# Optimization experiments

Hardware: AMD Instinct MI355X
Metric: run time of the kernel (lower is better)

The kernel has to match this reference:

```python
import jax, jax.numpy as jnp
import numpy as np

# ---- 4-wire quantum gate: RX(x_w + theta_w) per wire, CNOT ring, <Z_w> per wire ----
N_WIRES = 4
DIM = 2 ** N_WIRES  # 16 statevector amplitudes

def _cnot_perm_inv():
    # CNOTs (0,1),(1,2),(2,3),(3,0) applied sequentially permute computational basis states.
    # inv[j] = k such that basis state k maps to j; then psi_new = psi_old[inv].
    inv = np.zeros(DIM, dtype=np.int32)
    for k in range(DIM):
        b = [(k >> 3) & 1, (k >> 2) & 1, (k >> 1) & 1, k & 1]  # wire 0 = MSB
        b[1] ^= b[0]; b[2] ^= b[1]; b[3] ^= b[2]; b[0] ^= b[3]
        nk = (b[0] << 3) | (b[1] << 2) | (b[2] << 1) | b[3]
        inv[nk] = k
    return jnp.asarray(inv)

_PERM = _cnot_perm_inv()
# sign[k, w] = (-1)^{bit_w(k)} for PauliZ expectation on wire w
_ZSIGN = jnp.asarray(np.array([[1.0 - 2.0 * ((k >> (3 - w)) & 1) for w in range(N_WIRES)]
                               for k in range(DIM)], dtype=np.float32))  # [16, 4]

def _qgate(angles, theta):
    # angles: [B, 4]. Encoder RX(x_w) then trainable RX(theta_w) on the same wire = RX(x_w + theta_w).
    a = (angles + theta) * 0.5
    c, s = jnp.cos(a), jnp.sin(a)
    amp = jnp.stack([c + 0j, (-1j) * s], axis=-1)  # [B, 4, 2] per-wire RX|0> amplitudes
    # product state over 4 wires -> [B, 16]
    psi = jnp.einsum('bi,bj,bk,bl->bijkl', amp[:, 0], amp[:, 1], amp[:, 2], amp[:, 3]).reshape(-1, DIM)
    psi = psi[:, _PERM]  # CNOT ring (classical basis permutation)
    probs = jnp.real(psi * jnp.conj(psi))  # [B, 16]
    return probs @ _ZSIGN  # [B, 4] PauliZ expectations


def setup_inputs() -> dict:
    key = jax.random.key(0)
    T, B, D, H, Q = 256, 2048, 128, 4, 4
    ks = jax.random.split(key, 16)
    inp = {"inputs": jax.random.normal(ks[0], (T, B, D), dtype=jnp.float32)}
    bound = 1.0 / float(np.sqrt(D + H))  # torch Linear default init range
    for j, n in enumerate(["f", "i", "u", "o"]):
        inp["W" + n] = jax.random.uniform(ks[1 + j], (Q, D + H), jnp.float32, -bound, bound)
        inp["b" + n] = jax.random.uniform(ks[5 + j], (Q,), jnp.float32, -bound, bound)
        inp["th" + n] = jax.random.normal(ks[9 + j], (Q,), dtype=jnp.float32)  # trainable RX angles
    return inp


def reference(inputs, Wf, bf, Wi, bi, Wu, bu, Wo, bo, thf, thi, thu, tho):
    B = inputs.shape[1]
    H = N_WIRES  # hidden_dim == n_qubits == 4
    h0 = jnp.zeros((B, H), dtype=inputs.dtype)
    c0 = jnp.zeros((B, H), dtype=inputs.dtype)

    def step(carry, x):
        hx, cx = carry
        comb = jnp.concatenate([x, hx], axis=1)  # [B, D+H]
        f = jax.nn.sigmoid(_qgate(comb @ Wf.T + bf, thf))
        i = jax.nn.sigmoid(_qgate(comb @ Wi.T + bi, thi))
        g = jnp.tanh(_qgate(comb @ Wu.T + bu, thu))
        o = jax.nn.sigmoid(_qgate(comb @ Wo.T + bo, tho))
        cx = f * cx + i * g
        hx = o * jnp.tanh(cx)
        return (hx, cx), hx

    (hx, cx), stacked = jax.lax.scan(step, (h0, c0), inputs)
    return (stacked, hx, cx)
```

## Files before the change

kernel.cpp:

```cpp
#include <hip/hip_runtime.h>

#define TT 256
#define BB 2048
#define DIN 128
#define DWROW 132
#define INV2PI 0.15915494309189535f
#define LOG2E  1.4426950408889634f

__device__ __forceinline__ const float* rfl_ptr(const float* p) {
    unsigned long long u = (unsigned long long)p;
    unsigned lo = __builtin_amdgcn_readfirstlane((unsigned)u);
    unsigned hi = __builtin_amdgcn_readfirstlane((unsigned)(u >> 32));
    return (const float*)(((unsigned long long)hi << 32) | lo);
}

__device__ __forceinline__ float bperm(int byte_addr, float v) {
    return __int_as_float(__builtin_amdgcn_ds_bpermute(byte_addr, __float_as_int(v)));
}

__global__ __launch_bounds__(256) void qlstm_phase1(
    const float* __restrict__ x,
    const float* __restrict__ Wf, const float* __restrict__ bf, const float* __restrict__ thf,
    const float* __restrict__ Wi, const float* __restrict__ bi, const float* __restrict__ thi,
    const float* __restrict__ Wu, const float* __restrict__ bu, const float* __restrict__ thu,
    const float* __restrict__ Wo, const float* __restrict__ bo, const float* __restrict__ tho,
    float* __restrict__ Ax)
{
    __shared__ float xT[DIN][65];

    const int tid = threadIdx.x;
    const size_t tile = blockIdx.x;

    const float4* xg = (const float4*)x + tile * (64 * DIN / 4);
#pragma unroll
    for (int i = 0; i < 8; ++i) {
        int f   = i * 256 + tid;
        int row = f >> 5;
        int c4  = f & 31;
        float4 v = xg[f];
        xT[4 * c4 + 0][row] = v.x;
        xT[4 * c4 + 1][row] = v.y;
        xT[4 * c4 + 2][row] = v.z;
        xT[4 * c4 + 3][row] = v.w;
    }
    __syncthreads();

    const int wv   = tid >> 6;
    const int lane = tid & 63;

    const float* Wp  = (wv == 0) ? Wf  : (wv == 1) ? Wi  : (wv == 2) ? Wu  : Wo;
    const float* bp  = (wv == 0) ? bf  : (wv == 1) ? bi  : (wv == 2) ? bu  : bo;
    const float* thp = (wv == 0) ? thf : (wv == 1) ? thi : (wv == 2) ? thu : tho;
    const float* Wg  = rfl_ptr(Wp);
    const float* bg  = rfl_ptr(bp);
    const float* thg = rfl_ptr(thp);

    float acc0 = bg[0] + thg[0];
    float acc1 = bg[1] + thg[1];
    float acc2 = bg[2] + thg[2];
    float acc3 = bg[3] + thg[3];

#pragma unroll 8
    for (int j = 0; j < DIN; ++j) {
        float xv = xT[j][lane];
        acc0 = fmaf(xv, Wg[0 * DWROW + j], acc0);
        acc1 = fmaf(xv, Wg[1 * DWROW + j], acc1);
        acc2 = fmaf(xv, Wg[2 * DWROW + j], acc2);
        acc3 = fmaf(xv, Wg[3 * DWROW + j], acc3);
    }

    float4 o;
    o.x = acc0 * INV2PI; o.y = acc1 * INV2PI;
    o.z = acc2 * INV2PI; o.w = acc3 * INV2PI;
    ((float4*)Ax)[(tile * 64 + lane) * 4 + wv] = o;
}

__global__ __launch_bounds__(64) void qlstm_phase2(
    const float* __restrict__ Ax,
    const float* __restrict__ Wf, const float* __restrict__ Wi,
    const float* __restrict__ Wu, const float* __restrict__ Wo,
    float* __restrict__ out)
{
    const int gtid = blockIdx.x * 64 + threadIdx.x;
    const int lane = threadIdx.x & 63;
    const int sub  = gtid & 15;
    const int w    = sub & 3;
    const int g    = (sub >> 2) & 3;
    const int b    = gtid >> 4;

    const float* Wg = (g == 0) ? Wf : (g == 1) ? Wi : (g == 2) ? Wu : Wo;
    const float wh0 = Wg[w * DWROW + DIN + 0] * INV2PI;
    const float wh1 = Wg[w * DWROW + DIN + 1] * INV2PI;
    const float wh2 = Wg[w * DWROW + DIN + 2] * INV2PI;
    const float wh3 = Wg[w * DWROW + DIN + 3] * INV2PI;

    const bool  isU = (g == 2);
    const float Ac  = isU ? 1.0f : 0.0f;
    const float Bc  = isU ? -2.0f : 1.0f;
    const float Kc  = isU ? (2.0f * LOG2E) : (-LOG2E);

    const int gb  = (lane & ~3) << 2;
    const int az0 = gb, az1 = gb + 4, az2 = gb + 8, az3 = gb + 12;
    const int bb16 = (lane & ~15) << 2;
    const int af = bb16 + (w << 2);
    const int ai = af + 16;
    const int au = af + 32;
    const int ao = af + 48;

    const size_t S = (size_t)BB * 16;
    const float* ap = Ax + (size_t)b * 16 + sub;

    float a0 = ap[0 * S], a1 = ap[1 * S], a2 = ap[2 * S], a3 = ap[3 * S];

    float hv0 = 0.f, hv1 = 0.f, hv2 = 0.f, hv3 = 0.f;
    float cst = 0.f;
    float h   = 0.f;

    for (int t = 0; t < TT; ++t) {
        float ax = a0;
        a0 = a1; a1 = a2; a2 = a3;
        int tn = t + 4; if (tn > TT - 1) tn = TT - 1;
        a3 = ap[(size_t)tn * S];

        float ang = ax;
        ang = fmaf(hv0, wh0, ang);
        ang = fmaf(hv1, wh1, ang);
        ang = fmaf(hv2, wh2, ang);
        ang = fmaf(hv3, wh3, ang);
        float z = __builtin_amdgcn_cosf(ang);

        float z0 = bperm(az0, z);
        float z1 = bperm(az1, z);
        float z2 = bperm(az2, z);
        float z3 = bperm(az3, z);

        float c0    = z1 * z2 * z3;
        float p01   = z0 * z1;
        float p012  = p01 * z2;
        float p0123 = p012 * z3;
        float G = (w == 0) ? c0 : (w == 1) ? p01 : (w == 2) ? p012 : p0123;

        float e   = __builtin_amdgcn_exp2f(Kc * G);
        float act = fmaf(Bc, __builtin_amdgcn_rcpf(1.0f + e), Ac);

        float fg = bperm(af, act);
        float ig = bperm(ai, act);
        float ug = bperm(au, act);
        float og = bperm(ao, act);

        cst = fmaf(fg, cst, ig * ug);
        float ec = __builtin_amdgcn_exp2f((2.0f * LOG2E) * cst);
        float th = 1.0f - 2.0f * __builtin_amdgcn_rcpf(1.0f + ec);
        h = og * th;

        if (g == 0)
            out[(size_t)t * (BB * 4) + b * 4 + w] = h;

        hv0 = bperm(az0, h);
        hv1 = bperm(az1, h);
        hv2 = bperm(az2, h);
        hv3 = bperm(az3, h);
    }

    if (g == 0) {
        out[(size_t)TT * BB * 4 + b * 4 + w]          = h;
        out[(size_t)TT * BB * 4 + BB * 4 + b * 4 + w] = cst;
    }
}

extern "C" void kernel_launch(void* const* d_in, const int* in_sizes, int n_in,
                              void* d_out, int out_size, void* d_ws, size_t ws_size,
                              hipStream_t stream)
{
    const float* x   = (const float*)d_in[0];
    const float* Wf  = (const float*)d_in[1];
    const float* bf  = (const float*)d_in[2];
    const float* thf = (const float*)d_in[3];
    const float* Wi  = (const float*)d_in[4];
    const float* bi  = (const float*)d_in[5];
    const float* thi = (const float*)d_in[6];
    const float* Wu  = (const float*)d_in[7];
    const float* bu  = (const float*)d_in[8];
    const float* thu = (const float*)d_in[9];
    const float* Wo  = (const float*)d_in[10];
    const float* bo  = (const float*)d_in[11];
    const float* tho = (const float*)d_in[12];
    float* Ax   = (float*)d_ws;
    float* outp = (float*)d_out;

    qlstm_phase1<<<dim3((TT * BB) / 64), dim3(256), 0, stream>>>(
        x, Wf, bf, thf, Wi, bi, thi, Wu, bu, thu, Wo, bo, tho, Ax);
    qlstm_phase2<<<dim3((BB * 16) / 64), dim3(64), 0, stream>>>(
        Ax, Wf, Wi, Wu, Wo, outp);
}
```

Baseline: 470.4 us.

## Compute all four gates per thread in recurrence and use DPP broadcasts

The recurrent phase now assigns one thread per (batch, wire) and computes all four gates in that thread, instead of one thread per (batch, gate, wire). Cross-lane exchange moves from ds_bpermute to DPP quad broadcasts, and the gate-exchange permute step is removed entirely. This cuts the launched threads by four and removes LDS-path permute latency from the serial time loop. In exchange each thread does four times the cos, exp and rcp work, which lengthens the per-step dependency chain, and the number of waves available to hide latency drops.

```diff
diff --git a/kernel.cpp b/kernel.cpp
--- a/kernel.cpp
+++ b/kernel.cpp
@@ -14,8 +14,17 @@
     return (const float*)(((unsigned long long)hi << 32) | lo);
 }
 
-__device__ __forceinline__ float bperm(int byte_addr, float v) {
-    return __int_as_float(__builtin_amdgcn_ds_bpermute(byte_addr, __float_as_int(v)));
+#define DPP_BCAST(dst, src, j) \
+    dst = __int_as_float(__builtin_amdgcn_update_dpp( \
+        0, __float_as_int(src), (j) * 0x55, 0xF, 0xF, true))
+
+__device__ __forceinline__ float sigm(float x) {
+    float e = __builtin_amdgcn_exp2f(-LOG2E * x);
+    return __builtin_amdgcn_rcpf(1.0f + e);
+}
+__device__ __forceinline__ float tanh_f(float x) {
+    float e = __builtin_amdgcn_exp2f((2.0f * LOG2E) * x);
+    return 1.0f - 2.0f * __builtin_amdgcn_rcpf(1.0f + e);
 }
 
 __global__ __launch_bounds__(256) void qlstm_phase1(
@@ -82,90 +91,87 @@
     float* __restrict__ out)
 {
     const int gtid = blockIdx.x * 64 + threadIdx.x;
-    const int lane = threadIdx.x & 63;
-    const int sub  = gtid & 15;
-    const int w    = sub & 3;
-    const int g    = (sub >> 2) & 3;
-    const int b    = gtid >> 4;
-
-    const float* Wg = (g == 0) ? Wf : (g == 1) ? Wi : (g == 2) ? Wu : Wo;
-    const float wh0 = Wg[w * DWROW + DIN + 0] * INV2PI;
-    const float wh1 = Wg[w * DWROW + DIN + 1] * INV2PI;
-    const float wh2 = Wg[w * DWROW + DIN + 2] * INV2PI;
-    const float wh3 = Wg[w * DWROW + DIN + 3] * INV2PI;
-
-    const bool  isU = (g == 2);
-    const float Ac  = isU ? 1.0f : 0.0f;
-    const float Bc  = isU ? -2.0f : 1.0f;
-    const float Kc  = isU ? (2.0f * LOG2E) : (-LOG2E);
-
-    const int gb  = (lane & ~3) << 2;
-    const int az0 = gb, az1 = gb + 4, az2 = gb + 8, az3 = gb + 12;
-    const int bb16 = (lane & ~15) << 2;
-    const int af = bb16 + (w << 2);
-    const int ai = af + 16;
-    const int au = af + 32;
-    const int ao = af + 48;
+    const int w = gtid & 3;
+    const int b = gtid >> 2;
+
+    const float* Ws[4] = {Wf, Wi, Wu, Wo};
+    float wh[4][4];
+#pragma unroll
+    for (int g = 0; g < 4; ++g)
+#pragma unroll
+        for (int j = 0; j < 4; ++j)
+            wh[g][j] = Ws[g][w * DWROW + DIN + j] * INV2PI;
 
     const size_t S = (size_t)BB * 16;
-    const float* ap = Ax + (size_t)b * 16 + sub;
-
-    float a0 = ap[0 * S], a1 = ap[1 * S], a2 = ap[2 * S], a3 = ap[3 * S];
+    const float* ap = Ax + (size_t)b * 16 + w;
+
+    float ar[4][4];
+#pragma unroll
+    for (int d = 0; d < 4; ++d)
+#pragma unroll
+        for (int g = 0; g < 4; ++g)
+            ar[d][g] = ap[(size_t)d * S + g * 4];
 
     float hv0 = 0.f, hv1 = 0.f, hv2 = 0.f, hv3 = 0.f;
     float cst = 0.f;
     float h   = 0.f;
 
-    for (int t = 0; t < TT; ++t) {
-        float ax = a0;
-        a0 = a1; a1 = a2; a2 = a3;
-        int tn = t + 4; if (tn > TT - 1) tn = TT - 1;
-        a3 = ap[(size_t)tn * S];
-
-        float ang = ax;
-        ang = fmaf(hv0, wh0, ang);
-        ang = fmaf(hv1, wh1, ang);
-        ang = fmaf(hv2, wh2, ang);
-        ang = fmaf(hv3, wh3, ang);
-        float z = __builtin_amdgcn_cosf(ang);
-
-        float z0 = bperm(az0, z);
-        float z1 = bperm(az1, z);
-        float z2 = bperm(az2, z);
-        float z3 = bperm(az3, z);
-
-        float c0    = z1 * z2 * z3;
-        float p01   = z0 * z1;
-        float p012  = p01 * z2;
-        float p0123 = p012 * z3;
-        float G = (w == 0) ? c0 : (w == 1) ? p01 : (w == 2) ? p012 : p0123;
-
-        float e   = __builtin_amdgcn_exp2f(Kc * G);
-        float act = fmaf(Bc, __builtin_amdgcn_rcpf(1.0f + e), Ac);
-
-        float fg = bperm(af, act);
-        float ig = bperm(ai, act);
-        float ug = bperm(au, act);
-        float og = bperm(ao, act);
-
-        cst = fmaf(fg, cst, ig * ug);
-        float ec = __builtin_amdgcn_exp2f((2.0f * LOG2E) * cst);
-        float th = 1.0f - 2.0f * __builtin_amdgcn_rcpf(1.0f + ec);
-        h = og * th;
-
-        if (g == 0)
+    for (int t4 = 0; t4 < TT / 4; ++t4) {
+#pragma unroll
+        for (int k = 0; k < 4; ++k) {
+            const int t = 4 * t4 + k;
+            float a0 = ar[k][0], a1 = ar[k][1], a2 = ar[k][2], a3 = ar[k][3];
+            int tn = t + 4; if (tn > TT - 1) tn = TT - 1;
+#pragma unroll
+            for (int g = 0; g < 4; ++g)
+                ar[k][g] = ap[(size_t)tn * S + g * 4];
+
+            float z[4];
+#pragma unroll
+            for (int g = 0; g < 4; ++g) {
+                float ang = (g == 0) ? a0 : (g == 1) ? a1 : (g == 2) ? a2 : a3;
+                ang = fmaf(hv0, wh[g][0], ang);
+                ang = fmaf(hv1, wh[g][1], ang);
+                ang = fmaf(hv2, wh[g][2], ang);
+                ang = fmaf(hv3, wh[g][3], ang);
+                z[g] = __builtin_amdgcn_cosf(ang);
+            }
+
+            float G[4];
+#pragma unroll
+            for (int g = 0; g < 4; ++g) {
+                float q0, q1, q2, q3;
+                DPP_BCAST(q0, z[g], 0);
+                DPP_BCAST(q1, z[g], 1);
+                DPP_BCAST(q2, z[g], 2);
+                DPP_BCAST(q3, z[g], 3);
+                float p01   = q0 * q1;
+                float p012  = p01 * q2;
+                float p0123 = p012 * q3;
+                float c0    = q1 * q2 * q3;
+                G[g] = (w == 0) ? c0 : (w == 1) ? p01 : (w == 2) ? p012 : p0123;
+            }
+
+            float fg = sigm(G[0]);
+            float ig = sigm(G[1]);
+            float ug = tanh_f(G[2]);
+            float og = sigm(G[3]);
+
+            cst = fmaf(fg, cst, ig * ug);
+            float th = tanh_f(cst);
+            h = og * th;
+
             out[(size_t)t * (BB * 4) + b * 4 + w] = h;
 
-        hv0 = bperm(az0, h);
-        hv1 = bperm(az1, h);
-        hv2 = bperm(az2, h);
-        hv3 = bperm(az3, h);
+            DPP_BCAST(hv0, h, 0);
+            DPP_BCAST(hv1, h, 1);
+            DPP_BCAST(hv2, h, 2);
+            DPP_BCAST(hv3, h, 3);
+        }
     }
 
-    if (g == 0) {
-        out[(size_t)TT * BB * 4 + b * 4 + w]          = h;
-        out[(size_t)TT * BB * 4 + BB * 4 + b * 4 + w] = cst;
-    }
+    out[(size_t)TT * BB * 4 + b * 4 + w]          = h;
+    out[(size_t)TT * BB * 4 + BB * 4 + b * 4 + w] = cst;
 }
 
 extern "C" void kernel_launch(void* const* d_in, const int* in_sizes, int n_in,
@@ -190,6 +196,6 @@
 
     qlstm_phase1<<<dim3((TT * BB) / 64), dim3(256), 0, stream>>>(
         x, Wf, bf, thf, Wi, bi, thi, Wu, bu, thu, Wo, bo, tho, Ax);
-    qlstm_phase2<<<dim3((BB * 16) / 64), dim3(64), 0, stream>>>(
+    qlstm_phase2<<<dim3((BB * 4) / 64), dim3(64), 0, stream>>>(
         Ax, Wf, Wi, Wu, Wo, outp);
 }
```

New measurement: 469.8 us. No clear change (-0.1%).
